# Optimization experiments

Hardware: AMD Instinct MI355X
Metric: run time of the kernel (lower is better)

## Reference

```python
import jax, jax.numpy as jnp
import numpy as np

N_NODES = 163840
N_EDGES = 2621440
F_IN = 64
F_HID = 64
SUBG = 20  # size_subgraph_samples
NEG_SLOPE = 0.2


def gat_conv(x, src, dst, W, a_src, a_dst, b):
    """PyG GATConv, heads=1, concat. src/dst already include self-loops."""
    n = x.shape[0]
    h = x @ W                               # [N, H]
    al_s = h @ a_src                        # [N]
    al_d = h @ a_dst                        # [N]
    e = jax.nn.leaky_relu(al_s[src] + al_d[dst], NEG_SLOPE)  # [E]
    # softmax over incoming edges of each dst node
    m = jax.ops.segment_max(e, dst, num_segments=n)
    ex = jnp.exp(e - m[dst])
    denom = jax.ops.segment_sum(ex, dst, num_segments=n)
    alpha = ex / (denom[dst] + 1e-16)
    msg = h[src] * alpha[:, None]           # [E, H]
    out = jax.ops.segment_sum(msg, dst, num_segments=n)
    return out + b


def setup_inputs() -> dict:
    key = jax.random.key(0)
    ks = jax.random.split(key, 12)
    s = 0.05
    return {
        "x": jax.random.normal(ks[0], (N_NODES, F_IN), jnp.float32),
        "edge_index": jax.random.randint(ks[1], (2, N_EDGES), 0, N_NODES, jnp.int64 if jax.config.jax_enable_x64 else jnp.int32),
        "W1": jax.random.normal(ks[2], (F_IN, F_HID), jnp.float32) * s,
        "a_src1": jax.random.normal(ks[3], (F_HID,), jnp.float32) * s,
        "a_dst1": jax.random.normal(ks[4], (F_HID,), jnp.float32) * s,
        "b1": jnp.zeros((F_HID,), jnp.float32),
        "W2": jax.random.normal(ks[5], (F_HID, F_HID), jnp.float32) * s,
        "a_src2": jax.random.normal(ks[6], (F_HID,), jnp.float32) * s,
        "a_dst2": jax.random.normal(ks[7], (F_HID,), jnp.float32) * s,
        "b2": jnp.zeros((F_HID,), jnp.float32),
        "W_out": jax.random.normal(ks[8], (F_HID * SUBG, 1), jnp.float32) * s,
        "b_out": jnp.zeros((1,), jnp.float32),
    }


def reference(x, edge_index, W1, a_src1, a_dst1, b1, W2, a_src2, a_dst2, b2, W_out, b_out):
    n = x.shape[0]
    loop = jnp.arange(n, dtype=edge_index.dtype)
    src = jnp.concatenate([edge_index[0], loop])  # add_self_loops=True
    dst = jnp.concatenate([edge_index[1], loop])
    h = gat_conv(x, src, dst, W1, a_src1, a_dst1, b1)
    h = jax.nn.relu(h)  # dropout is identity in eval mode
    h = gat_conv(h, src, dst, W2, a_src2, a_dst2, b2)
    h = jax.nn.relu(h)
    h = h.reshape(n // SUBG, F_HID * SUBG)
    return h @ W_out + b_out
```

## Files before the change

kernel.cpp:

```cpp
#include <hip/hip_runtime.h>
#include <math.h>

#define F 64
#define NPB 160
#define BCAP 3584

typedef __attribute__((ext_vector_type(8))) short bf16x8;
typedef __attribute__((ext_vector_type(4))) float f32x4;

__device__ inline unsigned short f2bf(float f) {
  unsigned int u = __float_as_uint(f);
  u += 0x7fffu + ((u >> 16) & 1u);
  return (unsigned short)(u >> 16);
}

__global__ __launch_bounds__(256) void k_prep(const float* __restrict__ W1, const float* __restrict__ W2,
                                              uint4* __restrict__ wf, int* __restrict__ bcnt, int nb,
                                              float* __restrict__ out, const float* __restrict__ bo, int ng) {
  int tid = threadIdx.x;
  if (blockIdx.x == 0) {
    for (int i = tid; i < 1024; i += 256) {
      int layer = i >> 9, rem = i & 511;
      int cb = rem >> 6, lane = rem & 63;
      int c = cb >> 1, kk = cb & 1;
      int l15 = lane & 15, quad = lane >> 4;
      const float* W = layer ? W2 : W1;
      unsigned short p[8];
      #pragma unroll
      for (int j = 0; j < 8; j++) {
        int kd = kk * 32 + quad * 8 + j;
        p[j] = f2bf(W[kd * F + c * 16 + l15]);
      }
      wf[i] = *(const uint4*)p;
    }
  } else {
    for (int i = tid; i < nb * 16; i += 256) bcnt[i] = 0;
    float b0 = bo[0];
    for (int i = tid; i < ng; i += 256) out[i] = b0;
  }
}

__device__ __forceinline__ void gemm_body(const float* __restrict__ in, const uint4* __restrict__ wf,
                                          const float* __restrict__ avs, const float* __restrict__ avd,
                                          unsigned short* __restrict__ hgb, float* __restrict__ als,
                                          float* __restrict__ ald, int n, int bid, int nbl) {
  int tid = threadIdx.x, lane = tid & 63, wv = tid >> 6;
  int l15 = lane & 15, quad = lane >> 4;
  bf16x8 bfr[4][2];
  #pragma unroll
  for (int cb = 0; cb < 8; cb++) {
    uint4 u = wf[cb * 64 + lane];
    bfr[cb >> 1][cb & 1] = *(const bf16x8*)&u;
  }
  float as_l[4], ad_l[4];
  #pragma unroll
  for (int c = 0; c < 4; c++) { as_l[c] = avs[c * 16 + l15]; ad_l[c] = avd[c * 16 + l15]; }

  int nchunks = n >> 6;
  for (int chunk = bid; chunk < nchunks; chunk += nbl) {
    int r0 = (chunk << 6) + (wv << 4);
    bf16x8 a0, a1;
    const float4* xr = (const float4*)(in + (size_t)(r0 + l15) * F + quad * 8);
    float4 xa = xr[0], xb = xr[1];
    float4 xc = xr[8], xd = xr[9];
    a0[0] = (short)f2bf(xa.x); a0[1] = (short)f2bf(xa.y); a0[2] = (short)f2bf(xa.z); a0[3] = (short)f2bf(xa.w);
    a0[4] = (short)f2bf(xb.x); a0[5] = (short)f2bf(xb.y); a0[6] = (short)f2bf(xb.z); a0[7] = (short)f2bf(xb.w);
    a1[0] = (short)f2bf(xc.x); a1[1] = (short)f2bf(xc.y); a1[2] = (short)f2bf(xc.z); a1[3] = (short)f2bf(xc.w);
    a1[4] = (short)f2bf(xd.x); a1[5] = (short)f2bf(xd.y); a1[6] = (short)f2bf(xd.z); a1[7] = (short)f2bf(xd.w);
    f32x4 cfr[4];
    #pragma unroll
    for (int c = 0; c < 4; c++) {
      cfr[c] = (f32x4){0.f, 0.f, 0.f, 0.f};
      cfr[c] = __builtin_amdgcn_mfma_f32_16x16x32_bf16(a0, bfr[c][0], cfr[c], 0, 0, 0);
      cfr[c] = __builtin_amdgcn_mfma_f32_16x16x32_bf16(a1, bfr[c][1], cfr[c], 0, 0, 0);
    }
    #pragma unroll
    for (int i = 0; i < 4; i++) {
      int row = r0 + quad * 4 + i;
      #pragma unroll
      for (int c = 0; c < 4; c++) hgb[(size_t)row * F + c * 16 + l15] = f2bf(cfr[c][i]);
      float ps = cfr[0][i] * as_l[0] + cfr[1][i] * as_l[1] + cfr[2][i] * as_l[2] + cfr[3][i] * as_l[3];
      float pd = cfr[0][i] * ad_l[0] + cfr[1][i] * ad_l[1] + cfr[2][i] * ad_l[2] + cfr[3][i] * ad_l[3];
      #pragma unroll
      for (int o = 1; o <= 8; o <<= 1) { ps += __shfl_xor(ps, o); pd += __shfl_xor(pd, o); }
      if (l15 == 0) { als[row] = ps; ald[row] = pd; }
    }
  }
}

__global__ __launch_bounds__(256) void k_scatter_gemm1(const int* __restrict__ esrc, const int* __restrict__ edst,
                                                       int* __restrict__ bcnt, unsigned int* __restrict__ binned,
                                                       int e, int ch, int S,
                                                       const float* __restrict__ x, const uint4* __restrict__ wf,
                                                       const float* __restrict__ avs, const float* __restrict__ avd,
                                                       unsigned short* __restrict__ hgb, float* __restrict__ als,
                                                       float* __restrict__ ald, int n) {
  int k = blockIdx.x, tid = threadIdx.x;
  if (k < S) {
    __shared__ int hist[1024];
    __shared__ int cur[1024];
    for (int i = tid; i < 1024; i += 256) hist[i] = 0;
    __syncthreads();
    int beg = k * ch, end = min(e, beg + ch);
    int len = end - beg;
    if (len <= 0) return;
    int nv = len >> 2;
    for (int g = tid; g < nv; g += 256) {
      int4 d4 = *(const int4*)(edst + beg + (g << 2));
      atomicAdd(&hist[d4.x / NPB], 1);
      atomicAdd(&hist[d4.y / NPB], 1);
      atomicAdd(&hist[d4.z / NPB], 1);
      atomicAdd(&hist[d4.w / NPB], 1);
    }
    for (int i = beg + (nv << 2) + tid; i < end; i += 256) atomicAdd(&hist[edst[i] / NPB], 1);
    __syncthreads();
    for (int b = tid; b < 1024; b += 256) {
      int c = hist[b];
      int base = 0;
      if (c) base = atomicAdd(&bcnt[b * 16], c);
      cur[b] = b * BCAP + base;
    }
    __syncthreads();
    for (int g = tid; g < nv; g += 256) {
      int i = beg + (g << 2);
      int4 d4 = *(const int4*)(edst + i);
      int4 s4 = *(const int4*)(esrc + i);
      #pragma unroll
      for (int j = 0; j < 4; j++) {
        int d = (j == 0) ? d4.x : (j == 1) ? d4.y : (j == 2) ? d4.z : d4.w;
        int s = (j == 0) ? s4.x : (j == 1) ? s4.y : (j == 2) ? s4.z : s4.w;
        int b = d / NPB;
        int p = atomicAdd(&cur[b], 1);
        if (p < (b + 1) * BCAP) binned[p] = (unsigned int)s | ((unsigned int)(d - b * NPB) << 24);
      }
    }
    for (int i = beg + (nv << 2) + tid; i < end; i += 256) {
      int d = edst[i];
      int b = d / NPB;
      int p = atomicAdd(&cur[b], 1);
      if (p < (b + 1) * BCAP) binned[p] = (unsigned int)esrc[i] | ((unsigned int)(d - b * NPB) << 24);
    }
    return;
  }
  gemm_body(x, wf, avs, avd, hgb, als, ald, n, k - S, (int)gridDim.x - S);
}

__global__ __launch_bounds__(256) void k_csr_g2(const unsigned int* __restrict__ binned,
                                                const int* __restrict__ bcnt,
                                                int* __restrict__ ssrc, int* __restrict__ offs,
                                                const unsigned short* __restrict__ hgb,
                                                const float* __restrict__ als, const float* __restrict__ ald,
                                                const float* __restrict__ bias, const uint4* __restrict__ wf2,
                                                const float* __restrict__ avs, const float* __restrict__ avd,
                                                unsigned short* __restrict__ hgb2, float* __restrict__ als2,
                                                float* __restrict__ ald2, int n, int nb) {
  __shared__ int ncnt[NPB];
  __shared__ int noff[NPB];
  __shared__ int cur[NPB];
  __shared__ int wsum[4];
  __shared__ int stage[BCAP];
  __shared__ __align__(16) unsigned short hsh[NPB][72];
  int b = blockIdx.x, tid = threadIdx.x;
  int lane = tid & 63, wv = tid >> 6;
  int* red = stage;

  int acc = 0;
  for (int j = tid; j < b; j += 256) acc += min(bcnt[j * 16], BCAP);
  red[tid] = acc;
  __syncthreads();
  #pragma unroll
  for (int o = 128; o > 0; o >>= 1) {
    if (tid < o) red[tid] += red[tid + o];
    __syncthreads();
  }
  int outbase = red[0];
  int ecnt = min(bcnt[b * 16], BCAP);
  int node0 = b * NPB;
  int nn = min(NPB, n - node0);
  const uint4* bq = (const uint4*)(binned + (size_t)b * BCAP);
  int nv4 = ecnt >> 2;
  for (int i = tid; i < NPB; i += 256) ncnt[i] = 0;
  __syncthreads();
  for (int i = tid; i < nv4; i += 256) {
    uint4 q = bq[i];
    atomicAdd(&ncnt[q.x >> 24], 1);
    atomicAdd(&ncnt[q.y >> 24], 1);
    atomicAdd(&ncnt[q.z >> 24], 1);
    atomicAdd(&ncnt[q.w >> 24], 1);
  }
  for (int i = (nv4 << 2) + tid; i < ecnt; i += 256)
    atomicAdd(&ncnt[binned[(size_t)b * BCAP + i] >> 24], 1);
  __syncthreads();
  int v = (tid < nn) ? ncnt[tid] : 0;
  int x = v;
  #pragma unroll
  for (int o = 1; o <= 32; o <<= 1) { int y = __shfl_up(x, o); if (lane >= o) x += y; }
  if (lane == 63) wsum[wv] = x;
  __syncthreads();
  int add = 0;
  for (int w = 0; w < wv; w++) add += wsum[w];
  int incl = x + add;
  if (tid < nn) {
    int nf = incl - v;
    noff[tid] = nf;
    cur[tid] = nf;
    offs[node0 + tid] = outbase + nf;
  }
  __syncthreads();
  for (int i = tid; i < nv4; i += 256) {
    uint4 q = bq[i];
    int p0 = atomicAdd(&cur[q.x >> 24], 1); stage[p0] = (int)(q.x & 0xFFFFFFu);
    int p1 = atomicAdd(&cur[q.y >> 24], 1); stage[p1] = (int)(q.y & 0xFFFFFFu);
    int p2 = atomicAdd(&cur[q.z >> 24], 1); stage[p2] = (int)(q.z & 0xFFFFFFu);
    int p3 = atomicAdd(&cur[q.w >> 24], 1); stage[p3] = (int)(q.w & 0xFFFFFFu);
  }
  for (int i = (nv4 << 2) + tid; i < ecnt; i += 256) {
    unsigned int q = binned[(size_t)b * BCAP + i];
    int p = atomicAdd(&cur[q >> 24], 1);
    stage[p] = (int)(q & 0xFFFFFFu);
  }
  __syncthreads();
  for (int i = tid; i < ecnt; i += 256) ssrc[outbase + i] = stage[i];
  if (b == nb - 1 && tid == 0) offs[n] = outbase + ecnt;

  int g8 = lane >> 3, l8 = lane & 7;
  const uint4* hg4 = (const uint4*)hgb;
  float4 bl0 = ((const float4*)bias)[l8 * 2];
  float4 bl1 = ((const float4*)bias)[l8 * 2 + 1];

  for (int p = 0; p < 5; p++) {
    int row = p * 32 + wv * 8 + g8;
    int node = node0 + row;
    bool rowok = row < nn;
    int cnode = min(node, n - 1);
    int deg = rowok ? ncnt[row] : 0;
    int lbeg = rowok ? noff[row] : 0;
    float aldv = ald[cnode];

    float ts = als[cnode] + aldv;
    ts = fmaxf(ts, 0.2f * ts);
    float exs = __expf(ts);
    float s = exs;
    uint4 us = hg4[(size_t)cnode * 8 + l8];
    float acc8[8];
    acc8[0] = exs * __uint_as_float(us.x << 16);
    acc8[1] = exs * __uint_as_float(us.x & 0xffff0000u);
    acc8[2] = exs * __uint_as_float(us.y << 16);
    acc8[3] = exs * __uint_as_float(us.y & 0xffff0000u);
    acc8[4] = exs * __uint_as_float(us.z << 16);
    acc8[5] = exs * __uint_as_float(us.z & 0xffff0000u);
    acc8[6] = exs * __uint_as_float(us.w << 16);
    acc8[7] = exs * __uint_as_float(us.w & 0xffff0000u);

    #pragma unroll 4
    for (int j = 0; j < deg; j++) {
      int src = stage[lbeg + j];
      float t = als[src] + aldv;
      t = fmaxf(t, 0.2f * t);
      float ex = __expf(t);
      s += ex;
      uint4 u = hg4[(size_t)src * 8 + l8];
      acc8[0] = fmaf(ex, __uint_as_float(u.x << 16), acc8[0]);
      acc8[1] = fmaf(ex, __uint_as_float(u.x & 0xffff0000u), acc8[1]);
      acc8[2] = fmaf(ex, __uint_as_float(u.y << 16), acc8[2]);
      acc8[3] = fmaf(ex, __uint_as_float(u.y & 0xffff0000u), acc8[3]);
      acc8[4] = fmaf(ex, __uint_as_float(u.z << 16), acc8[4]);
      acc8[5] = fmaf(ex, __uint_as_float(u.z & 0xffff0000u), acc8[5]);
      acc8[6] = fmaf(ex, __uint_as_float(u.w << 16), acc8[6]);
      acc8[7] = fmaf(ex, __uint_as_float(u.w & 0xffff0000u), acc8[7]);
    }

    float iv = 1.f / (s + 1e-16f);
    float r[8];
    r[0] = fmaxf(fmaf(acc8[0], iv, bl0.x), 0.f);
    r[1] = fmaxf(fmaf(acc8[1], iv, bl0.y), 0.f);
    r[2] = fmaxf(fmaf(acc8[2], iv, bl0.z), 0.f);
    r[3] = fmaxf(fmaf(acc8[3], iv, bl0.w), 0.f);
    r[4] = fmaxf(fmaf(acc8[4], iv, bl1.x), 0.f);
    r[5] = fmaxf(fmaf(acc8[5], iv, bl1.y), 0.f);
    r[6] = fmaxf(fmaf(acc8[6], iv, bl1.z), 0.f);
    r[7] = fmaxf(fmaf(acc8[7], iv, bl1.w), 0.f);
    unsigned short pk[8];
    #pragma unroll
    for (int kk = 0; kk < 8; kk++) pk[kk] = f2bf(r[kk]);
    *(uint4*)&hsh[row][l8 * 8] = *(const uint4*)pk;
  }
  __syncthreads();

  int l15 = lane & 15, quad = lane >> 4;
  bf16x8 bfr[4][2];
  #pragma unroll
  for (int cb = 0; cb < 8; cb++) {
    uint4 u = wf2[cb * 64 + lane];
    bfr[cb >> 1][cb & 1] = *(const bf16x8*)&u;
  }
  float as_l[4], ad_l[4];
  #pragma unroll
  for (int c = 0; c < 4; c++) { as_l[c] = avs[c * 16 + l15]; ad_l[c] = avd[c * 16 + l15]; }

  #pragma unroll
  for (int t = 0; t < 3; t++) {
    int strip = t * 4 + wv;
    if (strip < 10) {
      int r0 = strip << 4;
      uint4 u0 = *(const uint4*)&hsh[r0 + l15][quad * 8];
      uint4 u1 = *(const uint4*)&hsh[r0 + l15][quad * 8 + 32];
      bf16x8 a0 = *(const bf16x8*)&u0;
      bf16x8 a1 = *(const bf16x8*)&u1;
      f32x4 cfr[4];
      #pragma unroll
      for (int c = 0; c < 4; c++) {
        cfr[c] = (f32x4){0.f, 0.f, 0.f, 0.f};
        cfr[c] = __builtin_amdgcn_mfma_f32_16x16x32_bf16(a0, bfr[c][0], cfr[c], 0, 0, 0);
        cfr[c] = __builtin_amdgcn_mfma_f32_16x16x32_bf16(a1, bfr[c][1], cfr[c], 0, 0, 0);
      }
      #pragma unroll
      for (int i = 0; i < 4; i++) {
        int row = node0 + r0 + quad * 4 + i;
        if (row < n) {
          #pragma unroll
          for (int c = 0; c < 4; c++) hgb2[(size_t)row * F + c * 16 + l15] = f2bf(cfr[c][i]);
        }
        float ps = cfr[0][i] * as_l[0] + cfr[1][i] * as_l[1] + cfr[2][i] * as_l[2] + cfr[3][i] * as_l[3];
        float pd = cfr[0][i] * ad_l[0] + cfr[1][i] * ad_l[1] + cfr[2][i] * ad_l[2] + cfr[3][i] * ad_l[3];
        #pragma unroll
        for (int o = 1; o <= 8; o <<= 1) { ps += __shfl_xor(ps, o); pd += __shfl_xor(pd, o); }
        if (l15 == 0 && row < n) { als2[row] = ps; ald2[row] = pd; }
      }
    }
  }
}

__device__ __forceinline__ void agg_node(int node, int n, const int* __restrict__ offs,
                                         const int* __restrict__ ssrc,
                                         const uint4* __restrict__ hg4,
                                         const float* __restrict__ als,
                                         const float* __restrict__ ald,
                                         float4 bl0, float4 bl1, int l8, float r[8]) {
  int cnode = min(node, n - 1);
  int beg = offs[cnode];
  int deg = offs[cnode + 1] - beg;
  float aldv = ald[cnode];

  float ts = als[cnode] + aldv;
  ts = fmaxf(ts, 0.2f * ts);
  float exs = __expf(ts);
  float s = exs;
  uint4 us = hg4[(size_t)cnode * 8 + l8];
  float acc[8];
  acc[0] = exs * __uint_as_float(us.x << 16);
  acc[1] = exs * __uint_as_float(us.x & 0xffff0000u);
  acc[2] = exs * __uint_as_float(us.y << 16);
  acc[3] = exs * __uint_as_float(us.y & 0xffff0000u);
  acc[4] = exs * __uint_as_float(us.z << 16);
  acc[5] = exs * __uint_as_float(us.z & 0xffff0000u);
  acc[6] = exs * __uint_as_float(us.w << 16);
  acc[7] = exs * __uint_as_float(us.w & 0xffff0000u);

  #pragma unroll 4
  for (int j = 0; j < deg; j++) {
    int src = ssrc[beg + j];
    float t = als[src] + aldv;
    t = fmaxf(t, 0.2f * t);
    float ex = __expf(t);
    s += ex;
    uint4 u = hg4[(size_t)src * 8 + l8];
    acc[0] = fmaf(ex, __uint_as_float(u.x << 16), acc[0]);
    acc[1] = fmaf(ex, __uint_as_float(u.x & 0xffff0000u), acc[1]);
    acc[2] = fmaf(ex, __uint_as_float(u.y << 16), acc[2]);
    acc[3] = fmaf(ex, __uint_as_float(u.y & 0xffff0000u), acc[3]);
    acc[4] = fmaf(ex, __uint_as_float(u.z << 16), acc[4]);
    acc[5] = fmaf(ex, __uint_as_float(u.z & 0xffff0000u), acc[5]);
    acc[6] = fmaf(ex, __uint_as_float(u.w << 16), acc[6]);
    acc[7] = fmaf(ex, __uint_as_float(u.w & 0xffff0000u), acc[7]);
  }

  float iv = 1.f / (s + 1e-16f);
  r[0] = fmaxf(fmaf(acc[0], iv, bl0.x), 0.f);
  r[1] = fmaxf(fmaf(acc[1], iv, bl0.y), 0.f);
  r[2] = fmaxf(fmaf(acc[2], iv, bl0.z), 0.f);
  r[3] = fmaxf(fmaf(acc[3], iv, bl0.w), 0.f);
  r[4] = fmaxf(fmaf(acc[4], iv, bl1.x), 0.f);
  r[5] = fmaxf(fmaf(acc[5], iv, bl1.y), 0.f);
  r[6] = fmaxf(fmaf(acc[6], iv, bl1.z), 0.f);
  r[7] = fmaxf(fmaf(acc[7], iv, bl1.w), 0.f);
}

__global__ __launch_bounds__(256) void k_spmm_out(const int* __restrict__ offs, const int* __restrict__ ssrc,
                                                  const unsigned short* __restrict__ hgb,
                                                  const float* __restrict__ als, const float* __restrict__ ald,
                                                  const float* __restrict__ bias, const float* __restrict__ Wout,
                                                  float* __restrict__ out, int n) {
  int tid = threadIdx.x, lane = tid & 63, wv = tid >> 6;
  int g8 = lane >> 3, l8 = lane & 7;
  const uint4* hg4 = (const uint4*)hgb;
  float4 bl0 = ((const float4*)bias)[l8 * 2];
  float4 bl1 = ((const float4*)bias)[l8 * 2 + 1];

  __shared__ float gsl[3];
  if (tid < 3) gsl[tid] = 0.f;

  int node = (blockIdx.x * 4 + wv) * 8 + g8;
  bool nodeok = node < n;
  int cnode = min(node, n - 1);
  float r[8];
  agg_node(node, n, offs, ssrc, hg4, als, ald, bl0, bl1, l8, r);

  int node0 = blockIdx.x * 32;
  int grp0 = node0 / 20;
  int grp = cnode / 20, slot = cnode - grp * 20;
  const float* wr = Wout + slot * F + l8 * 8;
  float dot = 0.f;
  #pragma unroll
  for (int k = 0; k < 8; k++) dot = fmaf(r[k], wr[k], dot);
  #pragma unroll
  for (int o = 1; o <= 4; o <<= 1) dot += __shfl_xor(dot, o);
  __syncthreads();
  if (nodeok && l8 == 0) atomicAdd(&gsl[grp - grp0], dot);
  __syncthreads();
  if (tid < 3) {
    float v = gsl[tid];
    if (v != 0.f) atomicAdd(out + grp0 + tid, v);
  }
}

extern "C" void kernel_launch(void* const* d_in, const int* in_sizes, int n_in,
                              void* d_out, int out_size, void* d_ws, size_t ws_size,
                              hipStream_t stream) {
  const float* x   = (const float*)d_in[0];
  const int*   ei  = (const int*)d_in[1];
  const float* W1  = (const float*)d_in[2];
  const float* as1 = (const float*)d_in[3];
  const float* ad1 = (const float*)d_in[4];
  const float* b1  = (const float*)d_in[5];
  const float* W2  = (const float*)d_in[6];
  const float* as2 = (const float*)d_in[7];
  const float* ad2 = (const float*)d_in[8];
  const float* b2  = (const float*)d_in[9];
  const float* Wo  = (const float*)d_in[10];
  const float* bo  = (const float*)d_in[11];
  float* out = (float*)d_out;

  const int N = in_sizes[0] / F;
  const int E = in_sizes[1] / 2;
  const int* esrc = ei;
  const int* edst = ei + E;

  size_t off = 0;
  auto alloc = [&](size_t bytes) -> void* {
    void* p = (char*)d_ws + off;
    off += (bytes + 255) & ~(size_t)255;
    return p;
  };
  unsigned short* hgb  = (unsigned short*)alloc((size_t)N * F * 2);
  unsigned short* hgb2 = (unsigned short*)alloc((size_t)N * F * 2);
  float* als  = (float*)alloc((size_t)N * 4);
  float* ald  = (float*)alloc((size_t)N * 4);
  float* als2 = (float*)alloc((size_t)N * 4);
  float* ald2 = (float*)alloc((size_t)N * 4);
  int* offs   = (int*)alloc((size_t)(N + 1) * 4);
  int* bcnt   = (int*)alloc((size_t)1024 * 16 * 4);
  int* ssrc   = (int*)alloc((size_t)(E + 64) * 4);
  unsigned int* binned = (unsigned int*)alloc((size_t)1024 * BCAP * 4);
  uint4* wf   = (uint4*)alloc(16384);
  (void)ws_size; (void)n_in; (void)out_size;

  const int NG = N / 20;
  const int NB = (N + NPB - 1) / NPB;
  const int S = 256;
  const int CH = (((E + S - 1) / S) + 3) & ~3;

  k_prep<<<2, 256, 0, stream>>>(W1, W2, wf, bcnt, NB, out, bo, NG);
  k_scatter_gemm1<<<S + (N >> 6), 256, 0, stream>>>(esrc, edst, bcnt, binned, E, CH, S,
                                                    x, wf, as1, ad1, hgb, als, ald, N);
  k_csr_g2<<<NB, 256, 0, stream>>>(binned, bcnt, ssrc, offs, hgb, als, ald, b1,
                                   wf + 512, as2, ad2, hgb2, als2, ald2, N, NB);
  k_spmm_out<<<(N >> 5), 256, 0, stream>>>(offs, ssrc, hgb2, als2, ald2, b2, Wo, out, N);
}
```

Baseline: 270.5 us.

## Stage binned edges in shared memory and write them contiguously per bin

The scatter phase now sorts each chunk's edges by destination bin in LDS, using a block-wide prefix scan over the bin histogram. Each wave then copies whole bins to global memory as contiguous runs, replacing the scattered per-edge global stores and giving more coalesced writes. The chunk size is capped so a chunk fits the 40KB staging buffer, and the number of scatter blocks is derived from that cap. The larger shared allocation is declared for every block, including the GEMM blocks, which can lower their occupancy.

```diff
diff --git a/kernel.cpp b/kernel.cpp
--- a/kernel.cpp
+++ b/kernel.cpp
@@ -4,6 +4,7 @@
 #define F 64
 #define NPB 160
 #define BCAP 3584
+#define CHMAX 10240
 
 typedef __attribute__((ext_vector_type(8))) short bf16x8;
 typedef __attribute__((ext_vector_type(4))) float f32x4;
@@ -95,10 +96,15 @@
                                                        const float* __restrict__ avs, const float* __restrict__ avd,
                                                        unsigned short* __restrict__ hgb, float* __restrict__ als,
                                                        float* __restrict__ ald, int n) {
+  __shared__ int hist[1024];
+  __shared__ int lboff[1024];
+  __shared__ int gbase[1024];
+  __shared__ int scur[1024];
+  __shared__ unsigned int stg[CHMAX];
+  __shared__ int wsum[4];
   int k = blockIdx.x, tid = threadIdx.x;
   if (k < S) {
-    __shared__ int hist[1024];
-    __shared__ int cur[1024];
+    int lane = tid & 63, wv = tid >> 6;
     for (int i = tid; i < 1024; i += 256) hist[i] = 0;
     __syncthreads();
     int beg = k * ch, end = min(e, beg + ch);
@@ -114,11 +120,26 @@
     }
     for (int i = beg + (nv << 2) + tid; i < end; i += 256) atomicAdd(&hist[edst[i] / NPB], 1);
     __syncthreads();
+    int b4 = tid * 4;
+    int c0 = hist[b4], c1 = hist[b4 + 1], c2 = hist[b4 + 2], c3 = hist[b4 + 3];
+    int csum = c0 + c1 + c2 + c3;
+    int xs = csum;
+    #pragma unroll
+    for (int o = 1; o <= 32; o <<= 1) { int y = __shfl_up(xs, o); if (lane >= o) xs += y; }
+    if (lane == 63) wsum[wv] = xs;
+    __syncthreads();
+    int add = 0;
+    for (int w = 0; w < wv; w++) add += wsum[w];
+    int excl = xs + add - csum;
+    lboff[b4] = excl;           scur[b4] = excl;
+    lboff[b4 + 1] = excl + c0;  scur[b4 + 1] = excl + c0;
+    lboff[b4 + 2] = excl + c0 + c1;       scur[b4 + 2] = excl + c0 + c1;
+    lboff[b4 + 3] = excl + c0 + c1 + c2;  scur[b4 + 3] = excl + c0 + c1 + c2;
     for (int b = tid; b < 1024; b += 256) {
       int c = hist[b];
       int base = 0;
       if (c) base = atomicAdd(&bcnt[b * 16], c);
-      cur[b] = b * BCAP + base;
+      gbase[b] = b * BCAP + base;
     }
     __syncthreads();
     for (int g = tid; g < nv; g += 256) {
@@ -130,15 +151,26 @@
         int d = (j == 0) ? d4.x : (j == 1) ? d4.y : (j == 2) ? d4.z : d4.w;
         int s = (j == 0) ? s4.x : (j == 1) ? s4.y : (j == 2) ? s4.z : s4.w;
         int b = d / NPB;
-        int p = atomicAdd(&cur[b], 1);
-        if (p < (b + 1) * BCAP) binned[p] = (unsigned int)s | ((unsigned int)(d - b * NPB) << 24);
+        int p = atomicAdd(&scur[b], 1);
+        stg[p] = (unsigned int)s | ((unsigned int)(d - b * NPB) << 24);
       }
     }
     for (int i = beg + (nv << 2) + tid; i < end; i += 256) {
       int d = edst[i];
       int b = d / NPB;
-      int p = atomicAdd(&cur[b], 1);
-      if (p < (b + 1) * BCAP) binned[p] = (unsigned int)esrc[i] | ((unsigned int)(d - b * NPB) << 24);
+      int p = atomicAdd(&scur[b], 1);
+      stg[p] = (unsigned int)esrc[i] | ((unsigned int)(d - b * NPB) << 24);
+    }
+    __syncthreads();
+    for (int b = wv; b < 1024; b += 4) {
+      int ln = hist[b];
+      int lb = lboff[b];
+      int gb = gbase[b];
+      int gend = (b + 1) * BCAP;
+      for (int t = lane; t < ln; t += 64) {
+        int d = gb + t;
+        if (d < gend) binned[d] = stg[lb + t];
+      }
     }
     return;
   }
@@ -467,7 +499,7 @@
 
   const int NG = N / 20;
   const int NB = (N + NPB - 1) / NPB;
-  const int S = 256;
+  const int S = (E + CHMAX - 1) / CHMAX;
   const int CH = (((E + S - 1) / S) + 3) & ~3;
 
   k_prep<<<2, 256, 0, stream>>>(W1, W2, wf, bcnt, NB, out, bo, NG);
```

After: 288.6 us. 6.7% more time.

## Use coarse 640-node scatter buckets and fixed-stride CSR with per-node degrees

Applied to the files above, without the earlier changes.

The edge scatter now bins edges into 256 coarse buckets of 640 destination nodes instead of 1024 buckets of 160, cutting shared-memory histogram size and global bucket atomics. Each CSR block reads its whole coarse bucket and filters out the edges for its 160-node slice. Source segments are stored at a fixed per-block stride, and a separate degree array replaces offset differences. This removes the block-prefix reduction over all bucket counts that every CSR block ran. In exchange each CSR block reads about four times as much binned data, and capacities are capped, so overflowing edges would be dropped.

```diff
diff --git a/kernel.cpp b/kernel.cpp
--- a/kernel.cpp
+++ b/kernel.cpp
@@ -3,7 +3,10 @@
 
 #define F 64
 #define NPB 160
-#define BCAP 3584
+#define CNB 640
+#define NBKC 256
+#define BCAPC 12288
+#define SSTR 3584
 
 typedef __attribute__((ext_vector_type(8))) short bf16x8;
 typedef __attribute__((ext_vector_type(4))) float f32x4;
@@ -15,7 +18,7 @@
 }
 
 __global__ __launch_bounds__(256) void k_prep(const float* __restrict__ W1, const float* __restrict__ W2,
-                                              uint4* __restrict__ wf, int* __restrict__ bcnt, int nb,
+                                              uint4* __restrict__ wf, int* __restrict__ bcnt,
                                               float* __restrict__ out, const float* __restrict__ bo, int ng) {
   int tid = threadIdx.x;
   if (blockIdx.x == 0) {
@@ -34,7 +37,7 @@
       wf[i] = *(const uint4*)p;
     }
   } else {
-    for (int i = tid; i < nb * 16; i += 256) bcnt[i] = 0;
+    for (int i = tid; i < NBKC * 16; i += 256) bcnt[i] = 0;
     float b0 = bo[0];
     for (int i = tid; i < ng; i += 256) out[i] = b0;
   }
@@ -97,9 +100,9 @@
                                                        float* __restrict__ ald, int n) {
   int k = blockIdx.x, tid = threadIdx.x;
   if (k < S) {
-    __shared__ int hist[1024];
-    __shared__ int cur[1024];
-    for (int i = tid; i < 1024; i += 256) hist[i] = 0;
+    __shared__ int hist[NBKC];
+    __shared__ int cur[NBKC];
+    if (tid < NBKC) hist[tid] = 0;
     __syncthreads();
     int beg = k * ch, end = min(e, beg + ch);
     int len = end - beg;
@@ -107,18 +110,18 @@
     int nv = len >> 2;
     for (int g = tid; g < nv; g += 256) {
       int4 d4 = *(const int4*)(edst + beg + (g << 2));
-      atomicAdd(&hist[d4.x / NPB], 1);
-      atomicAdd(&hist[d4.y / NPB], 1);
-      atomicAdd(&hist[d4.z / NPB], 1);
-      atomicAdd(&hist[d4.w / NPB], 1);
-    }
-    for (int i = beg + (nv << 2) + tid; i < end; i += 256) atomicAdd(&hist[edst[i] / NPB], 1);
+      atomicAdd(&hist[d4.x / CNB], 1);
+      atomicAdd(&hist[d4.y / CNB], 1);
+      atomicAdd(&hist[d4.z / CNB], 1);
+      atomicAdd(&hist[d4.w / CNB], 1);
+    }
+    for (int i = beg + (nv << 2) + tid; i < end; i += 256) atomicAdd(&hist[edst[i] / CNB], 1);
     __syncthreads();
-    for (int b = tid; b < 1024; b += 256) {
-      int c = hist[b];
+    if (tid < NBKC) {
+      int c = hist[tid];
       int base = 0;
-      if (c) base = atomicAdd(&bcnt[b * 16], c);
-      cur[b] = b * BCAP + base;
+      if (c) base = atomicAdd(&bcnt[tid * 16], c);
+      cur[tid] = tid * BCAPC + base;
     }
     __syncthreads();
     for (int g = tid; g < nv; g += 256) {
@@ -129,16 +132,16 @@
       for (int j = 0; j < 4; j++) {
         int d = (j == 0) ? d4.x : (j == 1) ? d4.y : (j == 2) ? d4.z : d4.w;
         int s = (j == 0) ? s4.x : (j == 1) ? s4.y : (j == 2) ? s4.z : s4.w;
-        int b = d / NPB;
+        int b = d / CNB;
         int p = atomicAdd(&cur[b], 1);
-        if (p < (b + 1) * BCAP) binned[p] = (unsigned int)s | ((unsigned int)(d - b * NPB) << 24);
+        if (p < (b + 1) * BCAPC) binned[p] = (unsigned int)s | ((unsigned int)(d - b * CNB) << 20);
       }
     }
     for (int i = beg + (nv << 2) + tid; i < end; i += 256) {
       int d = edst[i];
-      int b = d / NPB;
+      int b = d / CNB;
       int p = atomicAdd(&cur[b], 1);
-      if (p < (b + 1) * BCAP) binned[p] = (unsigned int)esrc[i] | ((unsigned int)(d - b * NPB) << 24);
+      if (p < (b + 1) * BCAPC) binned[p] = (unsigned int)esrc[i] | ((unsigned int)(d - b * CNB) << 20);
     }
     return;
   }
@@ -148,48 +151,42 @@
 __global__ __launch_bounds__(256) void k_csr_g2(const unsigned int* __restrict__ binned,
                                                 const int* __restrict__ bcnt,
                                                 int* __restrict__ ssrc, int* __restrict__ offs,
+                                                int* __restrict__ ndeg,
                                                 const unsigned short* __restrict__ hgb,
                                                 const float* __restrict__ als, const float* __restrict__ ald,
                                                 const float* __restrict__ bias, const uint4* __restrict__ wf2,
                                                 const float* __restrict__ avs, const float* __restrict__ avd,
                                                 unsigned short* __restrict__ hgb2, float* __restrict__ als2,
-                                                float* __restrict__ ald2, int n, int nb) {
+                                                float* __restrict__ ald2, int n) {
   __shared__ int ncnt[NPB];
   __shared__ int noff[NPB];
   __shared__ int cur[NPB];
   __shared__ int wsum[4];
-  __shared__ int stage[BCAP];
+  __shared__ int btot_sh;
+  __shared__ int stage[SSTR];
   __shared__ __align__(16) unsigned short hsh[NPB][72];
-  int b = blockIdx.x, tid = threadIdx.x;
+  int g = blockIdx.x, tid = threadIdx.x;
   int lane = tid & 63, wv = tid >> 6;
-  int* red = stage;
-
-  int acc = 0;
-  for (int j = tid; j < b; j += 256) acc += min(bcnt[j * 16], BCAP);
-  red[tid] = acc;
-  __syncthreads();
-  #pragma unroll
-  for (int o = 128; o > 0; o >>= 1) {
-    if (tid < o) red[tid] += red[tid + o];
-    __syncthreads();
-  }
-  int outbase = red[0];
-  int ecnt = min(bcnt[b * 16], BCAP);
-  int node0 = b * NPB;
+  int cb = g >> 2;
+  unsigned int lo = (unsigned int)((g & 3) * NPB);
+  int ec = min(bcnt[cb * 16], BCAPC);
+  int node0 = g * NPB;
   int nn = min(NPB, n - node0);
-  const uint4* bq = (const uint4*)(binned + (size_t)b * BCAP);
-  int nv4 = ecnt >> 2;
-  for (int i = tid; i < NPB; i += 256) ncnt[i] = 0;
+  const uint4* bq = (const uint4*)(binned + (size_t)cb * BCAPC);
+  int nv4 = ec >> 2;
+  if (tid < NPB) ncnt[tid] = 0;
   __syncthreads();
   for (int i = tid; i < nv4; i += 256) {
     uint4 q = bq[i];
-    atomicAdd(&ncnt[q.x >> 24], 1);
-    atomicAdd(&ncnt[q.y >> 24], 1);
-    atomicAdd(&ncnt[q.z >> 24], 1);
-    atomicAdd(&ncnt[q.w >> 24], 1);
-  }
-  for (int i = (nv4 << 2) + tid; i < ecnt; i += 256)
-    atomicAdd(&ncnt[binned[(size_t)b * BCAP + i] >> 24], 1);
+    unsigned int l0 = (q.x >> 20) - lo; if (l0 < NPB) atomicAdd(&ncnt[l0], 1);
+    unsigned int l1 = (q.y >> 20) - lo; if (l1 < NPB) atomicAdd(&ncnt[l1], 1);
+    unsigned int l2 = (q.z >> 20) - lo; if (l2 < NPB) atomicAdd(&ncnt[l2], 1);
+    unsigned int l3 = (q.w >> 20) - lo; if (l3 < NPB) atomicAdd(&ncnt[l3], 1);
+  }
+  for (int i = (nv4 << 2) + tid; i < ec; i += 256) {
+    unsigned int l0 = (binned[(size_t)cb * BCAPC + i] >> 20) - lo;
+    if (l0 < NPB) atomicAdd(&ncnt[l0], 1);
+  }
   __syncthreads();
   int v = (tid < nn) ? ncnt[tid] : 0;
   int x = v;
@@ -202,26 +199,30 @@
   int incl = x + add;
   if (tid < nn) {
     int nf = incl - v;
+    int capdeg = max(0, min(v, SSTR - nf));
     noff[tid] = nf;
     cur[tid] = nf;
-    offs[node0 + tid] = outbase + nf;
+    ncnt[tid] = capdeg;
+    offs[node0 + tid] = g * SSTR + nf;
+    ndeg[node0 + tid] = capdeg;
+    if (tid == nn - 1) btot_sh = min(incl, SSTR);
   }
   __syncthreads();
   for (int i = tid; i < nv4; i += 256) {
     uint4 q = bq[i];
-    int p0 = atomicAdd(&cur[q.x >> 24], 1); stage[p0] = (int)(q.x & 0xFFFFFFu);
-    int p1 = atomicAdd(&cur[q.y >> 24], 1); stage[p1] = (int)(q.y & 0xFFFFFFu);
-    int p2 = atomicAdd(&cur[q.z >> 24], 1); stage[p2] = (int)(q.z & 0xFFFFFFu);
-    int p3 = atomicAdd(&cur[q.w >> 24], 1); stage[p3] = (int)(q.w & 0xFFFFFFu);
-  }
-  for (int i = (nv4 << 2) + tid; i < ecnt; i += 256) {
-    unsigned int q = binned[(size_t)b * BCAP + i];
-    int p = atomicAdd(&cur[q >> 24], 1);
-    stage[p] = (int)(q & 0xFFFFFFu);
-  }
-  __syncthreads();
-  for (int i = tid; i < ecnt; i += 256) ssrc[outbase + i] = stage[i];
-  if (b == nb - 1 && tid == 0) offs[n] = outbase + ecnt;
+    unsigned int l0 = (q.x >> 20) - lo; if (l0 < NPB) { int p = atomicAdd(&cur[l0], 1); if (p < SSTR) stage[p] = (int)(q.x & 0xFFFFFu); }
+    unsigned int l1 = (q.y >> 20) - lo; if (l1 < NPB) { int p = atomicAdd(&cur[l1], 1); if (p < SSTR) stage[p] = (int)(q.y & 0xFFFFFu); }
+    unsigned int l2 = (q.z >> 20) - lo; if (l2 < NPB) { int p = atomicAdd(&cur[l2], 1); if (p < SSTR) stage[p] = (int)(q.z & 0xFFFFFu); }
+    unsigned int l3 = (q.w >> 20) - lo; if (l3 < NPB) { int p = atomicAdd(&cur[l3], 1); if (p < SSTR) stage[p] = (int)(q.w & 0xFFFFFu); }
+  }
+  for (int i = (nv4 << 2) + tid; i < ec; i += 256) {
+    unsigned int q = binned[(size_t)cb * BCAPC + i];
+    unsigned int l0 = (q >> 20) - lo;
+    if (l0 < NPB) { int p = atomicAdd(&cur[l0], 1); if (p < SSTR) stage[p] = (int)(q & 0xFFFFFu); }
+  }
+  __syncthreads();
+  int btot = btot_sh;
+  for (int i = tid; i < btot; i += 256) ssrc[(size_t)g * SSTR + i] = stage[i];
 
   int g8 = lane >> 3, l8 = lane & 7;
   const uint4* hg4 = (const uint4*)hgb;
@@ -290,9 +291,9 @@
   int l15 = lane & 15, quad = lane >> 4;
   bf16x8 bfr[4][2];
   #pragma unroll
-  for (int cb = 0; cb < 8; cb++) {
-    uint4 u = wf2[cb * 64 + lane];
-    bfr[cb >> 1][cb & 1] = *(const bf16x8*)&u;
+  for (int cb2 = 0; cb2 < 8; cb2++) {
+    uint4 u = wf2[cb2 * 64 + lane];
+    bfr[cb2 >> 1][cb2 & 1] = *(const bf16x8*)&u;
   }
   float as_l[4], ad_l[4];
   #pragma unroll
@@ -332,6 +333,7 @@
 }
 
 __device__ __forceinline__ void agg_node(int node, int n, const int* __restrict__ offs,
+                                         const int* __restrict__ ndeg,
                                          const int* __restrict__ ssrc,
                                          const uint4* __restrict__ hg4,
                                          const float* __restrict__ als,
@@ -339,7 +341,7 @@
                                          float4 bl0, float4 bl1, int l8, float r[8]) {
   int cnode = min(node, n - 1);
   int beg = offs[cnode];
-  int deg = offs[cnode + 1] - beg;
+  int deg = ndeg[cnode];
   float aldv = ald[cnode];
 
   float ts = als[cnode] + aldv;
@@ -386,7 +388,8 @@
   r[7] = fmaxf(fmaf(acc[7], iv, bl1.w), 0.f);
 }
 
-__global__ __launch_bounds__(256) void k_spmm_out(const int* __restrict__ offs, const int* __restrict__ ssrc,
+__global__ __launch_bounds__(256) void k_spmm_out(const int* __restrict__ offs, const int* __restrict__ ndeg,
+                                                  const int* __restrict__ ssrc,
                                                   const unsigned short* __restrict__ hgb,
                                                   const float* __restrict__ als, const float* __restrict__ ald,
                                                   const float* __restrict__ bias, const float* __restrict__ Wout,
@@ -404,7 +407,7 @@
   bool nodeok = node < n;
   int cnode = min(node, n - 1);
   float r[8];
-  agg_node(node, n, offs, ssrc, hg4, als, ald, bl0, bl1, l8, r);
+  agg_node(node, n, offs, ndeg, ssrc, hg4, als, ald, bl0, bl1, l8, r);
 
   int node0 = blockIdx.x * 32;
   int grp0 = node0 / 20;
@@ -459,21 +462,22 @@
   float* als2 = (float*)alloc((size_t)N * 4);
   float* ald2 = (float*)alloc((size_t)N * 4);
   int* offs   = (int*)alloc((size_t)(N + 1) * 4);
-  int* bcnt   = (int*)alloc((size_t)1024 * 16 * 4);
-  int* ssrc   = (int*)alloc((size_t)(E + 64) * 4);
-  unsigned int* binned = (unsigned int*)alloc((size_t)1024 * BCAP * 4);
+  int* ndeg   = (int*)alloc((size_t)N * 4);
+  int* bcnt   = (int*)alloc((size_t)NBKC * 16 * 4);
+  int* ssrc   = (int*)alloc((size_t)1024 * SSTR * 4);
+  unsigned int* binned = (unsigned int*)alloc((size_t)NBKC * BCAPC * 4);
   uint4* wf   = (uint4*)alloc(16384);
   (void)ws_size; (void)n_in; (void)out_size;
 
   const int NG = N / 20;
-  const int NB = (N + NPB - 1) / NPB;
+  const int NBLK = (N + NPB - 1) / NPB;
   const int S = 256;
   const int CH = (((E + S - 1) / S) + 3) & ~3;
 
-  k_prep<<<2, 256, 0, stream>>>(W1, W2, wf, bcnt, NB, out, bo, NG);
+  k_prep<<<2, 256, 0, stream>>>(W1, W2, wf, bcnt, out, bo, NG);
   k_scatter_gemm1<<<S + (N >> 6), 256, 0, stream>>>(esrc, edst, bcnt, binned, E, CH, S,
                                                     x, wf, as1, ad1, hgb, als, ald, N);
-  k_csr_g2<<<NB, 256, 0, stream>>>(binned, bcnt, ssrc, offs, hgb, als, ald, b1,
-                                   wf + 512, as2, ad2, hgb2, als2, ald2, N, NB);
-  k_spmm_out<<<(N >> 5), 256, 0, stream>>>(offs, ssrc, hgb2, als2, ald2, b2, Wo, out, N);
-}
+  k_csr_g2<<<NBLK, 256, 0, stream>>>(binned, bcnt, ssrc, offs, ndeg, hgb, als, ald, b1,
+                                     wf + 512, as2, ad2, hgb2, als2, ald2, N);
+  k_spmm_out<<<(N >> 5), 256, 0, stream>>>(offs, ndeg, ssrc, hgb2, als2, ald2, b2, Wo, out, N);
+}
```

Result: faster. 258.5 us (median of 2 runs) (-4.5%).
